# Optimization experiments

Measured on AMD Instinct MI355X. Metric: run time of the kernel, lower is better.

Reference implementation:

```python
import jax, jax.numpy as jnp
import numpy as np

N_NODES = 100000
N_EDGES = 1600000
N_RELS = 19
DIMS = [1, 128, 128, 64]  # in_degree feature -> dims


def setup_inputs() -> dict:
    key = jax.random.key(0)
    ks = jax.random.split(key, 12)
    src = jax.random.randint(ks[0], (N_EDGES,), 0, N_NODES, dtype=jnp.int64)
    dst = jax.random.randint(ks[1], (N_EDGES,), 0, N_NODES, dtype=jnp.int64)
    etypes = jax.random.randint(ks[2], (N_EDGES,), 0, N_RELS, dtype=jnp.int64)
    inp = {"src": src, "dst": dst, "etypes": etypes}
    for i, (din, dout) in enumerate(zip(DIMS[:-1], DIMS[1:])):
        s = 1.0 / np.sqrt(max(din, 1))
        inp[f"W{i}"] = jax.random.normal(ks[3 + 3 * i], (N_RELS, din, dout), jnp.float32) * s
        inp[f"Wloop{i}"] = jax.random.normal(ks[4 + 3 * i], (din, dout), jnp.float32) * s
        inp[f"b{i}"] = jnp.zeros((dout,), jnp.float32)
    inp["num_nodes"] = N_NODES
    return inp


def _rel_graph_conv(h, src, dst, etypes, W, Wloop, b, num_nodes, activation):
    # per-relation transform of every node: [N, R, dout]
    transformed = jnp.einsum('nd,rdo->nro', h, W)
    # gather message per edge by (src node, edge relation): [E, dout]
    msg = transformed[src, etypes]
    # scatter-sum to destination nodes
    agg = jax.ops.segment_sum(msg, dst, num_segments=num_nodes)
    out = agg + h @ Wloop + b
    if activation is not None:
        out = activation(out)
    return out


def reference(src, dst, etypes, W0, Wloop0, b0, W1, Wloop1, b1, W2, Wloop2, b2, num_nodes):
    # h = g.in_degrees().view(-1, 1).float()
    deg = jax.ops.segment_sum(jnp.ones_like(dst, dtype=jnp.float32), dst,
                              num_segments=num_nodes)
    h = deg[:, None]
    h = _rel_graph_conv(h, src, dst, etypes, W0, Wloop0, b0, num_nodes, jax.nn.relu)
    h = _rel_graph_conv(h, src, dst, etypes, W1, Wloop1, b1, num_nodes, jax.nn.relu)
    h = _rel_graph_conv(h, src, dst, etypes, W2, Wloop2, b2, num_nodes, None)
    return h
```

## Files before the change

### kernel.cpp

```cpp
#include <hip/hip_runtime.h>
#include <hip/hip_bf16.h>
#include <stdint.h>

#define N_NODES 100000
#define N_EDGES 1600000
#define N_RELS  19
#define NQ      4
#define QN      25000
#define QTILES  196
#define NBQ     98
#define NSB     (NQ * NBQ)
#define N_BUCK  (NQ * N_RELS)
#define NBIN    391
#define NGR     8
#define NBK8    (N_BUCK * NGR)
#define NBIN8   (NBIN * NGR)
#define NHC     (N_BUCK + NBIN)
#define NHC2    (2 * NHC)
#define MSGQ    460000
#define NCKQ    3700
#define NCK_TOT 14000
#define EPB     2048
#define S1B     782

typedef __attribute__((ext_vector_type(8))) short bf16x8;
typedef __attribute__((ext_vector_type(4))) float f32x4;
typedef __attribute__((ext_vector_type(4))) int   int4v;

__device__ __forceinline__ unsigned short f2bf(float x) {
  union { float f; unsigned u; } v; v.f = x;
  unsigned r = v.u + 0x7FFF + ((v.u >> 16) & 1);
  return (unsigned short)(r >> 16);
}
__device__ __forceinline__ float bf2f(unsigned short b) {
  union { unsigned u; float f; } v; v.u = ((unsigned)b) << 16; return v.f;
}

__global__ void k_prep_w(const float* W1, const float* W2,
                         const float* Wl1, const float* Wl2,
                         unsigned short* Wt1, unsigned short* Wt2,
                         unsigned short* Wtl1, unsigned short* Wtl2) {
  int i = blockIdx.x * 256 + threadIdx.x;
  const int s1 = N_RELS * 128 * 128;
  const int s2 = N_RELS * 64 * 128;
  const int s3 = 128 * 128;
  const int s4 = 64 * 128;
  if (i < s1) {
    int r = i / (128 * 128); int rem = i % (128 * 128);
    int n = rem / 128, k = rem % 128;
    Wt1[i] = f2bf(W1[((size_t)r * 128 + k) * 128 + n]);
  } else if (i < s1 + s2) {
    int j = i - s1;
    int r = j / (64 * 128); int rem = j % (64 * 128);
    int n = rem / 128, k = rem % 128;
    Wt2[j] = f2bf(W2[((size_t)r * 128 + k) * 64 + n]);
  } else if (i < s1 + s2 + s3) {
    int j = i - s1 - s2; int n = j / 128, k = j % 128;
    Wtl1[j] = f2bf(Wl1[k * 128 + n]);
  } else if (i < s1 + s2 + s3 + s4) {
    int j = i - s1 - s2 - s3; int n = j / 128, k = j % 128;
    Wtl2[j] = f2bf(Wl2[k * 64 + n]);
  }
}

__global__ void k_hist(const int* __restrict__ dst, const int* __restrict__ et,
                       int* __restrict__ bcount8, int* __restrict__ bincount8,
                       int* __restrict__ histAll) {
  __shared__ int hK[N_BUCK], hB[NBIN];
  __shared__ int sb[256];
  int t = threadIdx.x, g = blockIdx.x & (NGR - 1);
  for (int i = t; i < N_BUCK; i += 256) hK[i] = 0;
  for (int i = t; i < NBIN; i += 256) hB[i] = 0;
  __syncthreads();
  int e0 = blockIdx.x * EPB;
  for (int r = 0; r < EPB / 256; r++) {
    int e = e0 + r * 256 + t;
    if (e < N_EDGES) {
      int d = dst[e];
      atomicAdd(&hK[(d / QN) * N_RELS + et[e]], 1);
      atomicAdd(&hB[d >> 8], 1);
    }
  }
  __syncthreads();
  int* hout = histAll + (size_t)blockIdx.x * NHC2;
  for (int i = t; i < N_BUCK; i += 256) {
    hout[i] = hK[i];
    if (hK[i]) atomicAdd(&bcount8[i * NGR + g], hK[i]);
  }
  for (int i = t; i < NBIN; i += 256) {
    hout[N_BUCK + i] = hB[i];
    if (hB[i]) atomicAdd(&bincount8[i * NGR + g], hB[i]);
  }
  {
    int v0 = (2 * t < N_BUCK) ? hK[2 * t] : 0;
    int v1 = (2 * t + 1 < N_BUCK) ? hK[2 * t + 1] : 0;
    sb[t] = v0 + v1;
    __syncthreads();
    for (int s = 1; s < 256; s <<= 1) {
      int x = (t >= s) ? sb[t - s] : 0;
      __syncthreads();
      sb[t] += x;
      __syncthreads();
    }
    int base = sb[t] - v0 - v1;
    if (2 * t < N_BUCK) hout[NHC + 2 * t] = base;
    if (2 * t + 1 < N_BUCK) hout[NHC + 2 * t + 1] = base + v0;
    __syncthreads();
  }
  {
    int v0 = (2 * t < NBIN) ? hB[2 * t] : 0;
    int v1 = (2 * t + 1 < NBIN) ? hB[2 * t + 1] : 0;
    sb[t] = v0 + v1;
    __syncthreads();
    for (int s = 1; s < 256; s <<= 1) {
      int x = (t >= s) ? sb[t - s] : 0;
      __syncthreads();
      sb[t] += x;
      __syncthreads();
    }
    int base = sb[t] - v0 - v1;
    if (2 * t < NBIN) hout[NHC + N_BUCK + 2 * t] = base;
    if (2 * t + 1 < NBIN) hout[NHC + N_BUCK + 2 * t + 1] = base + v0;
  }
}

__global__ void k_scan0(const int* __restrict__ bcount8, const int* __restrict__ bincount8,
                        int* boff, int* bcur8, int* cbase, int* qcs, int* selfb,
                        int* binoff8, int* bincur8) {
  __shared__ int shK[NBK8];
  __shared__ int sb76[N_BUCK];
  __shared__ int sbs[N_BUCK];
  __shared__ int sh[512];
  int t = threadIdx.x;
  for (int i = t; i < NBK8; i += 512) shK[i] = bcount8[i];
  __syncthreads();
  if (t < N_BUCK) {
    int s = 0;
    for (int gg = 0; gg < NGR; gg++) s += shK[t * NGR + gg];
    sb76[t] = s;
  }
  __syncthreads();
  if (t == 0) {
    int a = 0, cb = 0;
    for (int q = 0; q < NQ; q++) {
      qcs[q] = cb;
      for (int r = 0; r < N_RELS; r++) {
        int b = q * N_RELS + r;
        boff[b] = a; sbs[b] = a; cbase[b] = cb;
        a += sb76[b]; cb += (sb76[b] + 127) >> 7;
      }
      selfb[q] = cb; cb += QTILES;
    }
    qcs[NQ] = cb;
    boff[N_BUCK] = a;
  }
  __syncthreads();
  for (int i = t; i < NBK8; i += 512) {
    int b = i >> 3, gg = i & (NGR - 1);
    int base = sbs[b];
    for (int k = 0; k < gg; k++) base += shK[b * NGR + k];
    bcur8[i] = base;
  }
  int vals[7];
  int i0 = t * 7;
  int loc = 0;
  for (int k = 0; k < 7; k++) {
    int i = i0 + k;
    int v = (i < NBIN8) ? bincount8[i] : 0;
    vals[k] = v; loc += v;
  }
  sh[t] = loc;
  __syncthreads();
  for (int s = 1; s < 512; s <<= 1) {
    int x = (t >= s) ? sh[t - s] : 0;
    __syncthreads();
    sh[t] += x;
    __syncthreads();
  }
  int run = sh[t] - loc;
  for (int k = 0; k < 7; k++) {
    int i = i0 + k;
    if (i < NBIN8) { binoff8[i] = run; bincur8[i] = run; run += vals[k]; }
  }
  if (t == 511) binoff8[NBIN8] = sh[511];
}

__launch_bounds__(256)
__global__ void k_scat1a(const int* __restrict__ src, const int* __restrict__ dst,
                         const int* __restrict__ et,
                         const int* __restrict__ histAll,
                         int* __restrict__ bcur8,
                         int* __restrict__ srcS, int* __restrict__ posE) {
  __shared__ int sortK[EPB];
  __shared__ int lK[N_BUCK], gKr[N_BUCK];
  int t = threadIdx.x, blk = blockIdx.x, g = blk & (NGR - 1);
  const int* hin = histAll + (size_t)blk * NHC2;
  for (int i = t; i < N_BUCK; i += 256) {
    int h = hin[i], l = hin[NHC + i];
    lK[i] = l;
    gKr[i] = h ? (atomicAdd(&bcur8[i * NGR + g], h) - l) : 0;
  }
  __syncthreads();
  int e0 = blk * EPB;
  int nval = min(EPB, N_EDGES - e0);
  for (int r = 0; r < EPB / 256; r++) {
    int e = e0 + r * 256 + t;
    if (e < N_EDGES) {
      int d = dst[e], rl = et[e], sv = src[e];
      int bk = (d / QN) * N_RELS + rl;
      int lrk = atomicAdd(&lK[bk], 1);
      sortK[lrk] = sv | (bk << 17);
      posE[e] = gKr[bk] + lrk;
    }
  }
  __syncthreads();
  for (int r = 0; r < EPB / 256; r++) {
    int s = r * 256 + t;
    if (s < nval) {
      int v = sortK[s];
      srcS[gKr[v >> 17] + s] = v & 0x1FFFF;
    }
  }
}

__launch_bounds__(256)
__global__ void k_scat1b(const int* __restrict__ src, const int* __restrict__ dst,
                         const int* __restrict__ et,
                         const int* __restrict__ posE,
                         const int* __restrict__ histAll,
                         int* __restrict__ bincur8,
                         int* __restrict__ stgA, int* __restrict__ stgB) {
  __shared__ int sortA[EPB], sortBv[EPB];
  __shared__ int lB[NBIN], gBr[NBIN];
  int t = threadIdx.x, blk = blockIdx.x, g = blk & (NGR - 1);
  const int* hin = histAll + (size_t)blk * NHC2;
  for (int i = t; i < NBIN; i += 256) {
    int h = hin[N_BUCK + i], l = hin[NHC + N_BUCK + i];
    lB[i] = l;
    gBr[i] = h ? (atomicAdd(&bincur8[i * NGR + g], h) - l) : 0;
  }
  __syncthreads();
  int e0 = blk * EPB;
  int nval = min(EPB, N_EDGES - e0);
  for (int r = 0; r < EPB / 256; r++) {
    int e = e0 + r * 256 + t;
    if (e < N_EDGES) {
      int d = dst[e], rl = et[e], sv = src[e];
      int gpos = posE[e];
      int bn = d >> 8;
      int lrb = atomicAdd(&lB[bn], 1);
      sortA[lrb] = gpos | (rl << 21) | ((bn & 63) << 26);
      sortBv[lrb] = sv | ((d & 255) << 17) | ((bn >> 6) << 25);
    }
  }
  __syncthreads();
  for (int r = 0; r < EPB / 256; r++) {
    int s = r * 256 + t;
    if (s < nval) {
      int a = sortA[s], b = sortBv[s];
      int bn = ((a >> 26) & 63) | (((b >> 25) & 7) << 6);
      int adr = gBr[bn] + s;
      stgA[adr] = a & 0x03FFFFFF;
      stgB[adr] = b & 0x01FFFFFF;
    }
  }
}

__global__ void k_cnt(const int* __restrict__ stgB, const int* __restrict__ binoff8,
                      int* __restrict__ ncount) {
  __shared__ int c[256];
  int b = blockIdx.x, t = threadIdx.x;
  c[t] = 0;
  __syncthreads();
  int lo = binoff8[b * NGR], hi = binoff8[b * NGR + NGR];
  for (int s = lo + t; s < hi; s += 256)
    atomicAdd(&c[(stgB[s] >> 17) & 255], 1);
  __syncthreads();
  int n = b * 256 + t;
  if (n < N_NODES) ncount[n] = c[t];
}

__global__ void k_scanA(const int* __restrict__ ncount, int* __restrict__ bsum) {
  __shared__ int sh[256];
  int b = blockIdx.x, t = threadIdx.x;
  int q = b / NBQ, bb = b % NBQ;
  int i = bb * 256 + t;
  int val = (i < QN) ? (ncount[q * QN + i] + 1) : 0;
  sh[t] = val;
  __syncthreads();
  for (int s = 128; s > 0; s >>= 1) {
    if (t < s) sh[t] += sh[t + s];
    __syncthreads();
  }
  if (t == 0) bsum[b] = sh[0];
}

__global__ void k_scanB(const int* bsum, int* bbase, int* nodeoff) {
  __shared__ int sh[NSB];
  int t = threadIdx.x;
  if (t < NSB) sh[t] = bsum[t];
  __syncthreads();
  if (t < NQ) {
    int a = 0;
    for (int i = 0; i < NBQ; i++) {
      int v = sh[t * NBQ + i]; sh[t * NBQ + i] = a; a += v;
    }
    nodeoff[(t + 1) * QN + t] = a;
  }
  __syncthreads();
  if (t < NSB) bbase[t] = sh[t];
}

__global__ void k_scanC(const int* __restrict__ ncount,
                        const int* __restrict__ bbase,
                        const int* __restrict__ boff,
                        int* __restrict__ nodeoff, int* __restrict__ ginv) {
  __shared__ int sh[256];
  int b = blockIdx.x, t = threadIdx.x;
  int q = b / NBQ, bb = b % NBQ;
  int i = bb * 256 + t;
  int val = (i < QN) ? (ncount[q * QN + i] + 1) : 0;
  sh[t] = val;
  __syncthreads();
  for (int s = 1; s < 256; s <<= 1) {
    int x = (t >= s) ? sh[t - s] : 0;
    __syncthreads();
    sh[t] += x;
    __syncthreads();
  }
  int excl = sh[t] - val + bbase[b];
  if (i < QN) {
    int n = q * QN + i;
    nodeoff[n + q] = excl;
    int qedges = boff[(q + 1) * N_RELS] - boff[q * N_RELS];
    ginv[(size_t)q * MSGQ + excl] = qedges + i;
  }
}

__global__ void k_scat2(const int* __restrict__ stgA, const int* __restrict__ stgB,
                        const int* __restrict__ binoff8,
                        const int* __restrict__ nodeoff,
                        const int* __restrict__ boff,
                        const int* __restrict__ ncount,
                        int* __restrict__ ginv, int* __restrict__ Rg) {
  __shared__ int cur[256];
  __shared__ int R[256][N_RELS];
  __shared__ int qe0s[NQ + 1];
  int b = blockIdx.x, t = threadIdx.x;
  if (t <= NQ) qe0s[t] = boff[t * N_RELS];
  int n = b * 256 + t;
  if (n < N_NODES) {
    int q = n / QN;
    cur[t] = nodeoff[n + q] + 1;
  }
#pragma unroll
  for (int r = 0; r < N_RELS; r++) R[t][r] = 0;
  __syncthreads();
  int lo = binoff8[b * NGR], hi = binoff8[b * NGR + NGR];
  for (int s = lo + t; s < hi; s += 256) {
    int a = stgA[s], bb = stgB[s];
    int dlow = (bb >> 17) & 255;
    int slot = atomicAdd(&cur[dlow], 1);
    int pos = a & 0x1FFFFF, rel = (a >> 21) & 31;
    int sv = bb & 0x1FFFF;
    int d = b * 256 + dlow;
    int q = d / QN;
    ginv[(size_t)q * MSGQ + slot] = pos - qe0s[q];
    atomicAdd(&R[dlow][rel], ncount[sv]);
  }
  __syncthreads();
  if (n < N_NODES) {
#pragma unroll
    for (int r = 0; r < N_RELS; r++)
      Rg[(size_t)r * N_NODES + n] = R[t][r];
  }
}

__launch_bounds__(256, 3)
__global__ void k_h1(const int* __restrict__ Rg, const int* __restrict__ ncount,
                     const float* __restrict__ W0, const float* __restrict__ Wl0,
                     const float* __restrict__ b0,
                     unsigned short* __restrict__ h1) {
  __shared__ float W0s[N_RELS * 128];
  __shared__ float wl[128], bb[128];
  __shared__ __align__(16) unsigned short Hs[128 * 128];
  int t = threadIdx.x, blk = blockIdx.x;
  for (int i = t; i < N_RELS * 128; i += 256) W0s[i] = W0[i];
  if (t < 128) { wl[t] = Wl0[t]; bb[t] = b0[t]; }
  __syncthreads();
  int n0 = blk * 128;
  int cnt = min(128, N_NODES - n0);
  int ln = t >> 1;
  int half = (t & 1) * 64;
  if (ln < cnt) {
    int n = n0 + ln;
    float rr[N_RELS];
#pragma unroll
    for (int r = 0; r < N_RELS; r++) rr[r] = (float)Rg[(size_t)r * N_NODES + n];
    float dn = (float)ncount[n];
    for (int c0 = half; c0 < half + 64; c0 += 8) {
      float acc[8];
#pragma unroll
      for (int j = 0; j < 8; j++) acc[j] = dn * wl[c0 + j] + bb[c0 + j];
      for (int r = 0; r < N_RELS; r++) {
#pragma unroll
        for (int j = 0; j < 8; j++)
          acc[j] += rr[r] * W0s[r * 128 + c0 + j];
      }
      unsigned vs[4];
#pragma unroll
      for (int j = 0; j < 4; j++) {
        float x0 = fmaxf(acc[2 * j], 0.f), x1 = fmaxf(acc[2 * j + 1], 0.f);
        vs[j] = (unsigned)f2bf(x0) | ((unsigned)f2bf(x1) << 16);
      }
      int4v o = {(int)vs[0], (int)vs[1], (int)vs[2], (int)vs[3]};
      *(int4v*)&Hs[ln * 128 + c0] = o;
    }
  }
  __syncthreads();
  int tot = cnt * 16;
  for (int task = t; task < tot; task += 256)
    *(int4v*)&h1[(size_t)n0 * 128 + task * 8] = *(const int4v*)&Hs[task * 8];
}

__global__ void k_fill(const int* boff, const int* cbase,
                       const int* selfb, int* cA, int* cB) {
  int b = blockIdx.x;
  if (b < N_BUCK) {
    int cnt = boff[b + 1] - boff[b], e0 = boff[b], w0 = cbase[b];
    int rel = b % N_RELS;
    int nch = (cnt + 127) >> 7;
    for (int i = threadIdx.x; i < nch; i += blockDim.x) {
      cA[w0 + i] = (e0 + i * 128) | (rel << 21);
      cB[w0 + i] = min(128, cnt - i * 128);
    }
  } else {
    int q = b - N_BUCK;
    int w0 = selfb[q];
    for (int i = threadIdx.x; i < QTILES; i += blockDim.x) {
      cA[w0 + i] = (i * 128) | (19 << 21);
      cB[w0 + i] = min(128, QN - i * 128);
    }
  }
}

template <int NOUT>
__launch_bounds__(256, NOUT == 64 ? 6 : 4)
__global__ void k_gemm_msg(const unsigned short* __restrict__ hprev,
                           const unsigned short* __restrict__ Wt,
                           const unsigned short* __restrict__ Wtl,
                           const int* __restrict__ qcs, int q,
                           const int* __restrict__ cA,
                           const int* __restrict__ cB,
                           const int* __restrict__ srcS,
                           const int* __restrict__ boff,
                           unsigned short* __restrict__ msg) {
  const int LDK = 136;
  __shared__ __align__(16) unsigned short Bs[NOUT * LDK];

  int cs = qcs[q], ce = qcs[q + 1];
  int w = blockIdx.x;
  if (w >= ce - cs) return;
  w += cs;
  int pa = cA[w];
  int e0 = pa & 0x1FFFFF, rel = pa >> 21;
  int cnt = cB[w];
  bool self = (rel == 19);
  const unsigned short* wsrc = self ? Wtl : (Wt + (size_t)rel * NOUT * 128);
  int qe0 = boff[q * N_RELS];
  int qedges = boff[(q + 1) * N_RELS] - qe0;
  int ppos0 = self ? (qedges + e0) : (e0 - qe0);
  int tid = threadIdx.x;
  const int lane = tid & 63, wid = tid >> 6;

  int rowg[2]; bool valv[2];
#pragma unroll
  for (int fi = 0; fi < 2; fi++) {
    int m = wid * 32 + fi * 16 + (lane & 15);
    bool v = m < cnt;
    valv[fi] = v;
    int row = 0;
    if (v) row = self ? (q * QN + e0 + m) : srcS[e0 + m];
    rowg[fi] = row;
  }
  bf16x8 a[2][4];
#pragma unroll
  for (int fi = 0; fi < 2; fi++) {
    const unsigned short* rp = hprev + (size_t)rowg[fi] * 128 + (lane >> 4) * 8;
#pragma unroll
    for (int kk = 0; kk < 4; kk++)
      a[fi][kk] = *(const bf16x8*)&rp[kk * 32];
  }
#pragma unroll
  for (int fi = 0; fi < 2; fi++)
    if (!valv[fi]) {
#pragma unroll
      for (int kk = 0; kk < 4; kk++)
        a[fi][kk] = (bf16x8){0, 0, 0, 0, 0, 0, 0, 0};
    }

  for (int task = tid; task < NOUT * 16; task += 256) {
    int n = task >> 4, c = task & 15;
    *(int4v*)&Bs[n * LDK + c * 8] = *(const int4v*)&wsrc[n * 128 + c * 8];
  }
  __syncthreads();

  const int FJ = NOUT / 16;
  f32x4 acc[2][FJ];
#pragma unroll
  for (int i = 0; i < 2; i++)
#pragma unroll
    for (int j = 0; j < FJ; j++) acc[i][j] = (f32x4){0.f, 0.f, 0.f, 0.f};

#pragma unroll
  for (int kk = 0; kk < 4; kk++) {
    int kof = kk * 32 + (lane >> 4) * 8;
    bf16x8 b[FJ];
#pragma unroll
    for (int fj = 0; fj < FJ; fj++)
      b[fj] = *(const bf16x8*)&Bs[(fj * 16 + (lane & 15)) * LDK + kof];
#pragma unroll
    for (int fi = 0; fi < 2; fi++)
#pragma unroll
      for (int fj = 0; fj < FJ; fj++)
        acc[fi][fj] = __builtin_amdgcn_mfma_f32_16x16x32_bf16(a[fi][kk], b[fj], acc[fi][fj], 0, 0, 0);
  }

  __syncthreads();
  unsigned short* Cs = Bs;
#pragma unroll
  for (int fi = 0; fi < 2; fi++)
#pragma unroll
    for (int fj = 0; fj < FJ; fj++)
#pragma unroll
      for (int j = 0; j < 4; j++) {
        int mrow = wid * 32 + fi * 16 + (lane >> 4) * 4 + j;
        int col = fj * 16 + (lane & 15);
        Cs[mrow * NOUT + col] = f2bf(acc[fi][fj][j]);
      }
  __syncthreads();
  const int CW = NOUT / 8;
  for (int task = tid; task < cnt * CW; task += 256) {
    int row = task / CW, c = task % CW;
    *(int4v*)&msg[(size_t)(ppos0 + row) * NOUT + c * 8] =
        *(const int4v*)&Cs[row * NOUT + c * 8];
  }
}

template <int NOUT>
__global__ void k_reduce(const unsigned short* __restrict__ msg,
                         const int* __restrict__ ginv,
                         const int* __restrict__ nodeoff, int q,
                         const float* __restrict__ bias, int do_relu,
                         unsigned short* __restrict__ outh,
                         float* __restrict__ outf) {
  int t = threadIdx.x;
  int rn = blockIdx.x * 8 + (t >> 5);
  if (rn >= QN) return;
  int n = q * QN + rn;
  int l = t & 31;
  int lo = nodeoff[n + q], hi = nodeoff[n + q + 1];
  const int* gv = ginv + (size_t)q * MSGQ;
  if (NOUT == 128) {
    float a0 = 0.f, a1 = 0.f, a2 = 0.f, a3 = 0.f;
    for (int i = lo; i < hi; i++) {
      int ppos = gv[i];
      uint2 v = *(const uint2*)&msg[(size_t)ppos * 128 + l * 4];
      a0 += bf2f((unsigned short)(v.x & 0xffff));
      a1 += bf2f((unsigned short)(v.x >> 16));
      a2 += bf2f((unsigned short)(v.y & 0xffff));
      a3 += bf2f((unsigned short)(v.y >> 16));
    }
    a0 += bias[l * 4];     a1 += bias[l * 4 + 1];
    a2 += bias[l * 4 + 2]; a3 += bias[l * 4 + 3];
    if (do_relu) {
      a0 = fmaxf(a0, 0.f); a1 = fmaxf(a1, 0.f);
      a2 = fmaxf(a2, 0.f); a3 = fmaxf(a3, 0.f);
    }
    uint2 o;
    o.x = (unsigned)f2bf(a0) | ((unsigned)f2bf(a1) << 16);
    o.y = (unsigned)f2bf(a2) | ((unsigned)f2bf(a3) << 16);
    *(uint2*)&outh[(size_t)n * 128 + l * 4] = o;
  } else {
    float a0 = 0.f, a1 = 0.f;
    for (int i = lo; i < hi; i++) {
      int ppos = gv[i];
      unsigned v = *(const unsigned*)&msg[(size_t)ppos * 64 + l * 2];
      a0 += bf2f((unsigned short)(v & 0xffff));
      a1 += bf2f((unsigned short)(v >> 16));
    }
    a0 += bias[l * 2];
    a1 += bias[l * 2 + 1];
    if (do_relu) { a0 = fmaxf(a0, 0.f); a1 = fmaxf(a1, 0.f); }
    outf[(size_t)n * 64 + l * 2]     = a0;
    outf[(size_t)n * 64 + l * 2 + 1] = a1;
  }
}

extern "C" void kernel_launch(void* const* d_in, const int* in_sizes, int n_in,
                              void* d_out, int out_size, void* d_ws, size_t ws_size,
                              hipStream_t stream) {
  const int* src = (const int*)d_in[0];
  const int* dst = (const int*)d_in[1];
  const int* et  = (const int*)d_in[2];
  const float* W0  = (const float*)d_in[3];
  const float* Wl0 = (const float*)d_in[4];
  const float* b0  = (const float*)d_in[5];
  const float* W1  = (const float*)d_in[6];
  const float* Wl1 = (const float*)d_in[7];
  const float* b1  = (const float*)d_in[8];
  const float* W2  = (const float*)d_in[9];
  const float* Wl2 = (const float*)d_in[10];
  const float* b2  = (const float*)d_in[11];

  char* ws = (char*)d_ws;
  size_t off = 0;
  auto alloc = [&](size_t bytes) {
    void* p = ws + off;
    off = (off + bytes + 255) & ~(size_t)255;
    return p;
  };
  unsigned short* msg = (unsigned short*)alloc((size_t)MSGQ * 128 * 2);
  unsigned short* h1 = (unsigned short*)alloc((size_t)N_NODES * 128 * 2);
  unsigned short* h2 = (unsigned short*)alloc((size_t)N_NODES * 128 * 2);
  int* srcS = (int*)alloc((size_t)N_EDGES * 4);
  int* stgA = (int*)alloc((size_t)N_EDGES * 4);
  int* stgB = (int*)alloc((size_t)N_EDGES * 4);
  int* posE = (int*)alloc((size_t)N_EDGES * 4);
  int* ginv = (int*)alloc((size_t)NQ * MSGQ * 4);
  int* Rg   = (int*)alloc((size_t)N_RELS * N_NODES * 4);
  int* ncount  = (int*)alloc((size_t)N_NODES * 4);
  int* nodeoff = (int*)alloc((size_t)(N_NODES + NQ + 4) * 4);
  int* histAll = (int*)alloc((size_t)S1B * NHC2 * 4);
  unsigned short* Wt1  = (unsigned short*)alloc((size_t)N_RELS * 128 * 128 * 2);
  unsigned short* Wt2  = (unsigned short*)alloc((size_t)N_RELS * 64 * 128 * 2);
  unsigned short* Wtl1 = (unsigned short*)alloc((size_t)128 * 128 * 2);
  unsigned short* Wtl2 = (unsigned short*)alloc((size_t)64 * 128 * 2);
  int* acc0 = (int*)alloc((size_t)(NBK8 + NBIN8) * 4);
  int* bcount8   = acc0;
  int* bincount8 = acc0 + NBK8;
  int* ints = (int*)alloc(4096);
  int* boff   = ints;
  int* cbase  = ints + 80;
  int* qcs    = ints + 160;
  int* selfb  = ints + 168;
  int* bcur8  = (int*)alloc((size_t)NBK8 * 4);
  int* binoff8 = (int*)alloc((size_t)(NBIN8 + 1) * 4);
  int* bincur8 = (int*)alloc((size_t)NBIN8 * 4);
  int* bsum  = (int*)alloc((size_t)NSB * 4);
  int* bbase = (int*)alloc((size_t)NSB * 4);
  int* cA = (int*)alloc((size_t)NCK_TOT * 4);
  int* cB = (int*)alloc((size_t)NCK_TOT * 4);

  hipMemsetAsync(acc0, 0, (size_t)(NBK8 + NBIN8) * 4, stream);

  k_prep_w<<<1920, 256, 0, stream>>>(W1, W2, Wl1, Wl2, Wt1, Wt2, Wtl1, Wtl2);
  k_hist<<<S1B, 256, 0, stream>>>(dst, et, bcount8, bincount8, histAll);
  k_scan0<<<1, 512, 0, stream>>>(bcount8, bincount8, boff, bcur8, cbase, qcs,
                                 selfb, binoff8, bincur8);
  k_scat1a<<<S1B, 256, 0, stream>>>(src, dst, et, histAll, bcur8, srcS, posE);
  k_scat1b<<<S1B, 256, 0, stream>>>(src, dst, et, posE, histAll, bincur8,
                                    stgA, stgB);
  k_cnt<<<NBIN, 256, 0, stream>>>(stgB, binoff8, ncount);
  k_scanA<<<NSB, 256, 0, stream>>>(ncount, bsum);
  k_scanB<<<1, 512, 0, stream>>>(bsum, bbase, nodeoff);
  k_scanC<<<NSB, 256, 0, stream>>>(ncount, bbase, boff, nodeoff, ginv);
  k_scat2<<<NBIN, 256, 0, stream>>>(stgA, stgB, binoff8, nodeoff, boff,
                                    ncount, ginv, Rg);
  k_fill<<<N_BUCK + NQ, 256, 0, stream>>>(boff, cbase, selfb, cA, cB);
  k_h1<<<(N_NODES + 127) / 128, 256, 0, stream>>>(Rg, ncount, W0, Wl0, b0, h1);

  for (int q = 0; q < NQ; q++) {
    k_gemm_msg<128><<<NCKQ, 256, 0, stream>>>(h1, Wt1, Wtl1, qcs, q, cA, cB,
                                              srcS, boff, msg);
    k_reduce<128><<<QN / 8, 256, 0, stream>>>(msg, ginv, nodeoff, q, b1, 1,
                                              h2, nullptr);
  }
  for (int q = 0; q < NQ; q++) {
    k_gemm_msg<64><<<NCKQ, 256, 0, stream>>>(h2, Wt2, Wtl2, qcs, q, cA, cB,
                                             srcS, boff, msg);
    k_reduce<64><<<QN / 8, 256, 0, stream>>>(msg, ginv, nodeoff, q, b2, 0,
                                             nullptr, (float*)d_out);
  }
}
```

Before: 713.9 us.

## Swizzle GEMM LDS layout, split scat2 bins across two blocks, raise occupancy

Replaces the padded LDS row stride in k_gemm_msg with an XOR swizzle over unpadded rows. This shrinks shared memory per block and is meant to avoid bank conflicts on B-fragment reads and C-tile writes. The 128-wide variant's launch bound rises from 4 to 5 blocks per SM. k_scat2 now uses twice as many blocks, each owning half of a bin's 256 destination nodes, to cut LDS usage and add parallelism. The cost is that every edge in a bin is read twice, once by each half-block.

```diff
diff --git a/kernel.cpp b/kernel.cpp
--- a/kernel.cpp
+++ b/kernel.cpp
@@ -34,6 +34,9 @@
 }
 __device__ __forceinline__ float bf2f(unsigned short b) {
   union { unsigned u; float f; } v; v.u = ((unsigned)b) << 16; return v.f;
+}
+__device__ __forceinline__ int swz(int row, int col, int LD) {
+  return (row * LD + col) ^ (((row & 3) << 4) | ((row & 4) << 1));
 }
 
 __global__ void k_prep_w(const float* W1, const float* W2,
@@ -343,33 +346,39 @@
                         const int* __restrict__ boff,
                         const int* __restrict__ ncount,
                         int* __restrict__ ginv, int* __restrict__ Rg) {
-  __shared__ int cur[256];
-  __shared__ int R[256][N_RELS];
+  __shared__ int cur[128];
+  __shared__ int R[128][N_RELS];
   __shared__ int qe0s[NQ + 1];
-  int b = blockIdx.x, t = threadIdx.x;
+  int b2 = blockIdx.x, t = threadIdx.x;
+  int b = b2 >> 1, half = b2 & 1;
   if (t <= NQ) qe0s[t] = boff[t * N_RELS];
-  int n = b * 256 + t;
-  if (n < N_NODES) {
-    int q = n / QN;
-    cur[t] = nodeoff[n + q] + 1;
-  }
-#pragma unroll
-  for (int r = 0; r < N_RELS; r++) R[t][r] = 0;
+  int n = b * 256 + half * 128 + t;
+  if (t < 128) {
+    if (n < N_NODES) {
+      int q = n / QN;
+      cur[t] = nodeoff[n + q] + 1;
+    }
+#pragma unroll
+    for (int r = 0; r < N_RELS; r++) R[t][r] = 0;
+  }
   __syncthreads();
   int lo = binoff8[b * NGR], hi = binoff8[b * NGR + NGR];
   for (int s = lo + t; s < hi; s += 256) {
     int a = stgA[s], bb = stgB[s];
     int dlow = (bb >> 17) & 255;
-    int slot = atomicAdd(&cur[dlow], 1);
-    int pos = a & 0x1FFFFF, rel = (a >> 21) & 31;
-    int sv = bb & 0x1FFFF;
-    int d = b * 256 + dlow;
-    int q = d / QN;
-    ginv[(size_t)q * MSGQ + slot] = pos - qe0s[q];
-    atomicAdd(&R[dlow][rel], ncount[sv]);
-  }
-  __syncthreads();
-  if (n < N_NODES) {
+    if ((dlow >> 7) == half) {
+      int li = dlow & 127;
+      int slot = atomicAdd(&cur[li], 1);
+      int pos = a & 0x1FFFFF, rel = (a >> 21) & 31;
+      int sv = bb & 0x1FFFF;
+      int d = b * 256 + dlow;
+      int q = d / QN;
+      ginv[(size_t)q * MSGQ + slot] = pos - qe0s[q];
+      atomicAdd(&R[li][rel], ncount[sv]);
+    }
+  }
+  __syncthreads();
+  if (t < 128 && n < N_NODES) {
 #pragma unroll
     for (int r = 0; r < N_RELS; r++)
       Rg[(size_t)r * N_NODES + n] = R[t][r];
@@ -445,7 +454,7 @@
 }
 
 template <int NOUT>
-__launch_bounds__(256, NOUT == 64 ? 6 : 4)
+__launch_bounds__(256, NOUT == 64 ? 6 : 5)
 __global__ void k_gemm_msg(const unsigned short* __restrict__ hprev,
                            const unsigned short* __restrict__ Wt,
                            const unsigned short* __restrict__ Wtl,
@@ -455,8 +464,7 @@
                            const int* __restrict__ srcS,
                            const int* __restrict__ boff,
                            unsigned short* __restrict__ msg) {
-  const int LDK = 136;
-  __shared__ __align__(16) unsigned short Bs[NOUT * LDK];
+  __shared__ __align__(16) unsigned short Bs[NOUT * 128];
 
   int cs = qcs[q], ce = qcs[q + 1];
   int w = blockIdx.x;
@@ -501,7 +509,7 @@
 
   for (int task = tid; task < NOUT * 16; task += 256) {
     int n = task >> 4, c = task & 15;
-    *(int4v*)&Bs[n * LDK + c * 8] = *(const int4v*)&wsrc[n * 128 + c * 8];
+    *(int4v*)&Bs[swz(n, c * 8, 128)] = *(const int4v*)&wsrc[n * 128 + c * 8];
   }
   __syncthreads();
 
@@ -518,7 +526,7 @@
     bf16x8 b[FJ];
 #pragma unroll
     for (int fj = 0; fj < FJ; fj++)
-      b[fj] = *(const bf16x8*)&Bs[(fj * 16 + (lane & 15)) * LDK + kof];
+      b[fj] = *(const bf16x8*)&Bs[swz(fj * 16 + (lane & 15), kof, 128)];
 #pragma unroll
     for (int fi = 0; fi < 2; fi++)
 #pragma unroll
@@ -527,7 +535,6 @@
   }
 
   __syncthreads();
-  unsigned short* Cs = Bs;
 #pragma unroll
   for (int fi = 0; fi < 2; fi++)
 #pragma unroll
@@ -536,14 +543,14 @@
       for (int j = 0; j < 4; j++) {
         int mrow = wid * 32 + fi * 16 + (lane >> 4) * 4 + j;
         int col = fj * 16 + (lane & 15);
-        Cs[mrow * NOUT + col] = f2bf(acc[fi][fj][j]);
+        Bs[swz(mrow, col, NOUT)] = f2bf(acc[fi][fj][j]);
       }
   __syncthreads();
   const int CW = NOUT / 8;
   for (int task = tid; task < cnt * CW; task += 256) {
     int row = task / CW, c = task % CW;
     *(int4v*)&msg[(size_t)(ppos0 + row) * NOUT + c * 8] =
-        *(const int4v*)&Cs[row * NOUT + c * 8];
+        *(const int4v*)&Bs[swz(row, c * 8, NOUT)];
   }
 }
 
@@ -665,8 +672,8 @@
   k_scanA<<<NSB, 256, 0, stream>>>(ncount, bsum);
   k_scanB<<<1, 512, 0, stream>>>(bsum, bbase, nodeoff);
   k_scanC<<<NSB, 256, 0, stream>>>(ncount, bbase, boff, nodeoff, ginv);
-  k_scat2<<<NBIN, 256, 0, stream>>>(stgA, stgB, binoff8, nodeoff, boff,
-                                    ncount, ginv, Rg);
+  k_scat2<<<2 * NBIN, 256, 0, stream>>>(stgA, stgB, binoff8, nodeoff, boff,
+                                        ncount, ginv, Rg);
   k_fill<<<N_BUCK + NQ, 256, 0, stream>>>(boff, cbase, selfb, cA, cB);
   k_h1<<<(N_NODES + 127) / 128, 256, 0, stream>>>(Rg, ncount, W0, Wl0, b0, h1);
 
```

After: 1.072 ms. +50.2%, slower.
